# Kernel optimization log

Hardware: AMD Instinct MI355X
Metric: run time of the kernel (lower is better)

## Reference

```python
import jax, jax.numpy as jnp
import numpy as np

BITS = 4
VALS_PER_WORD = 4  # four 4-bit nibbles packed per 16-bit word


def dequantize(w_packed, w_scale, w_bias, dtype):
    # w_packed: [out, groups, cols] int32, each word holds 4 nibbles (little-endian)
    out, g, cols = w_packed.shape
    shifts = jnp.arange(VALS_PER_WORD, dtype=jnp.int32) * BITS  # [4]
    # [out, groups, cols, 4] nibble values in [0, 15]
    q = (w_packed[..., None] >> shifts) & 0xF
    q = q.astype(dtype).reshape(out, g, cols * VALS_PER_WORD)
    w = q * w_scale + w_bias  # per-group affine dequant, scale/bias broadcast over group
    return w.reshape(out, g * cols * VALS_PER_WORD)  # [out, in]


def setup_inputs() -> dict:
    key = jax.random.key(0)
    k1, k2, k3, k4, k5 = jax.random.split(key, 5)
    B, S, IN, OUT, G = 2, 2048, 4096, 16384, 16
    cols = IN // G // VALS_PER_WORD  # 64 packed words per group
    return {
        "input": jax.random.normal(k1, (B, S, IN), dtype=jnp.float32),
        "w_packed": jax.random.randint(k2, (OUT, G, cols), 0, 65536, dtype=jnp.int32),
        "w_scale": jax.random.uniform(k3, (OUT, G, 1), dtype=jnp.float32) * 0.01,
        "w_bias": jax.random.normal(k4, (OUT, G, 1), dtype=jnp.float32) * 0.05,
        "bias": jax.random.normal(k5, (OUT,), dtype=jnp.float32),
    }


def reference(input, w_packed, w_scale, w_bias, bias):
    weight = dequantize(w_packed, w_scale, w_bias, input.dtype)  # [out, in]
    # F.linear: y = x @ W^T + b
    return jnp.einsum("bsi,oi->bso", input, weight) + bias
```

## Files before the change

### kernel.cpp

```cpp
#include <hip/hip_runtime.h>
#include <hip/hip_bf16.h>


typedef short bf16x8 __attribute__((ext_vector_type(8)));
typedef float f32x4 __attribute__((ext_vector_type(4)));
typedef int i32x4 __attribute__((ext_vector_type(4)));
typedef unsigned short u16;
typedef unsigned short u16x8 __attribute__((ext_vector_type(8)));

#define BM 128
#define BN 128
#define BK 64
#define THREADS 256

static __device__ __forceinline__ u16 f2bf(float f) {
    __hip_bfloat16 h = __float2bfloat16(f);
    return __builtin_bit_cast(u16, h);
}


__global__ void rowstat_kernel(const float* __restrict__ x, float* __restrict__ sx,
                               float* __restrict__ rsx, int K) {
    const int m = blockIdx.x;
    const int l = threadIdx.x;
    const float4* p = (const float4*)(x + (size_t)m * K);
    float mx = 0.f;
    for (int i = l; i < (K >> 2); i += 64) {
        const float4 v = p[i];
        mx = fmaxf(mx, fmaxf(fmaxf(fabsf(v.x), fabsf(v.y)),
                             fmaxf(fabsf(v.z), fabsf(v.w))));
    }
    #pragma unroll
    for (int o = 32; o; o >>= 1) mx = fmaxf(mx, __shfl_xor(mx, o));
    if (l == 0) {
        mx = fmaxf(mx, 1e-20f);
        sx[m]  = mx * (1.f / 127.f);
        rsx[m] = 127.f / mx;
    }
}

__global__ void quantX_kernel(const float* __restrict__ x, const float* __restrict__ rsx,
                              char* __restrict__ xq, int kshift, size_t n16) {
    size_t i = (size_t)blockIdx.x * blockDim.x + threadIdx.x;
    if (i >= n16) return;
    const int m = (int)((i * 16) >> kshift);
    const float r = rsx[m];
    const float4* px = (const float4*)(x + i * 16);
    int out[4];
    #pragma unroll
    for (int w = 0; w < 4; ++w) {
        const float4 v = px[w];
        const int b0 = __float2int_rn(v.x * r) & 0xFF;
        const int b1 = __float2int_rn(v.y * r) & 0xFF;
        const int b2 = __float2int_rn(v.z * r) & 0xFF;
        const int b3 = __float2int_rn(v.w * r) & 0xFF;
        out[w] = b0 | (b1 << 8) | (b2 << 16) | (b3 << 24);
    }
    *(int4*)(xq + i * 16) = make_int4(out[0], out[1], out[2], out[3]);
}

__global__ void rowscaleW_kernel(const float* __restrict__ Ws,
                                 const float* __restrict__ Wb,
                                 float* __restrict__ swr, float* __restrict__ rswr,
                                 int G, int N) {
    const int n = blockIdx.x * blockDim.x + threadIdx.x;
    if (n >= N) return;
    float mx = 1e-20f;
    for (int g = 0; g < G; ++g) {
        const float s = Ws[(size_t)n * G + g];
        const float b = Wb[(size_t)n * G + g];
        mx = fmaxf(mx, fmaxf(fabsf(b), fabsf(fmaf(15.f, s, b))));
    }
    swr[n]  = mx * (1.f / 127.f);
    rswr[n] = 127.f / mx;
}

__global__ void quantW_row_kernel(const int* __restrict__ Wp, const float* __restrict__ Ws,
                                  const float* __restrict__ Wb, const float* __restrict__ rswr,
                                  char* __restrict__ wq, int K, int G, int gshift,
                                  int kcshift, size_t nthr) {
    size_t t = (size_t)blockIdx.x * blockDim.x + threadIdx.x;
    if (t >= nthr) return;
    const int n  = (int)(t >> kcshift);
    const int kc = (int)(t & ((1u << kcshift) - 1));
    const int g  = (kc << 4) >> gshift;
    const float s = Ws[(size_t)n * G + g];
    const float b = Wb[(size_t)n * G + g];
    const float rs = rswr[n];
    const int4 wv = *(const int4*)(Wp + (size_t)n * (K >> 2) + ((size_t)kc << 2));
    const int wds[4] = {wv.x, wv.y, wv.z, wv.w};
    int out[4];
    #pragma unroll
    for (int w = 0; w < 4; ++w) {
        int o = 0;
        #pragma unroll
        for (int j = 0; j < 4; ++j) {
            const float v = fmaf((float)((wds[w] >> (4 * j)) & 0xF), s, b);
            o |= (__float2int_rn(v * rs) & 0xFF) << (8 * j);
        }
        out[w] = o;
    }
    *(int4*)(wq + t * 16) = make_int4(out[0], out[1], out[2], out[3]);
}


__global__ __launch_bounds__(512, 2)
void gql_gemm_i8s(const char* __restrict__ xq,
                  const char* __restrict__ wq,
                  const float* __restrict__ swr,
                  const float* __restrict__ sx,
                  const float* __restrict__ Bias,
                  float* __restrict__ Out,
                  int M, int N, int K)
{
    __shared__ __align__(16) char sA[2][256 * 128];
    __shared__ __align__(16) char sB[2][256 * 128];

    const int tid  = threadIdx.x;
    const int lane = tid & 63;
    const int wid  = tid >> 6;
    const int wm   = wid >> 2;
    const int wn   = wid & 3;

    const int nwg = gridDim.x;
    int wg = blockIdx.x;
    if ((nwg & 7) == 0) wg = (wg & 7) * (nwg >> 3) + (wg >> 3);
    const int nt = N / 256;
    const int m0 = (wg / nt) * 256;
    const int n0 = (wg % nt) * 256;

    const int st_row = lane >> 3;
    const int st_g   = ((lane & 7) ^ (lane >> 3)) << 4;

    const int fr = lane & 15;
    const int fq = lane >> 4;

    i32x4 acc[8][4] = {};

    const int NT = K >> 7;

    auto stage = [&](int t, int buf) {
        const size_t k0 = (size_t)t << 7;
        #pragma unroll
        for (int i = 0; i < 4; ++i) {
            const int r = wid * 32 + i * 8 + st_row;
            const char* srcA = xq + (size_t)(m0 + r) * K + k0 + st_g;
            __builtin_amdgcn_global_load_lds(
                (const __attribute__((address_space(1))) void*)srcA,
                (__attribute__((address_space(3))) void*)&sA[buf][(wid * 32 + i * 8) * 128],
                16, 0, 0);
            const char* srcB = wq + (size_t)(n0 + r) * K + k0 + st_g;
            __builtin_amdgcn_global_load_lds(
                (const __attribute__((address_space(1))) void*)srcB,
                (__attribute__((address_space(3))) void*)&sB[buf][(wid * 32 + i * 8) * 128],
                16, 0, 0);
        }
    };

    auto ldsrd = [&](const char* base, int row, int gr) -> i32x4 {
        const u16x8 raw = *(const u16x8*)(base + row * 128 + gr * 16);
        return __builtin_bit_cast(i32x4, raw);
    };

    auto compute = [&](int buf) {
        #pragma unroll
        for (int kk = 0; kk < 2; ++kk) {
            const int gr = (kk * 4 + fq) ^ (fr & 7);
            i32x4 af[8], bfr[4];
            #pragma unroll
            for (int i = 0; i < 8; ++i)
                af[i] = ldsrd(&sA[buf][0], wm * 128 + i * 16 + fr, gr);
            #pragma unroll
            for (int j = 0; j < 4; ++j)
                bfr[j] = ldsrd(&sB[buf][0], wn * 64 + j * 16 + fr, gr);
            __builtin_amdgcn_s_setprio(1);
            #pragma unroll
            for (int i = 0; i < 8; ++i)
                #pragma unroll
                for (int j = 0; j < 4; ++j)
                    acc[i][j] = __builtin_amdgcn_mfma_i32_16x16x64_i8(
                        af[i], bfr[j], acc[i][j], 0, 0, 0);
            __builtin_amdgcn_s_setprio(0);
        }
    };

    stage(0, 0);
    int cur = 0;
    for (int t = 0; t < NT - 1; ++t) {
        stage(t + 1, cur ^ 1);
        __builtin_amdgcn_sched_barrier(0);
        asm volatile("s_waitcnt vmcnt(8)" ::: "memory");
        __builtin_amdgcn_s_barrier();
        asm volatile("" ::: "memory");
        compute(cur);
        __builtin_amdgcn_sched_barrier(0);
        asm volatile("" ::: "memory");
        __builtin_amdgcn_s_barrier();
        asm volatile("" ::: "memory");
        cur ^= 1;
    }
    asm volatile("s_waitcnt vmcnt(0)" ::: "memory");
    __builtin_amdgcn_s_barrier();
    asm volatile("" ::: "memory");
    compute(cur);

    #pragma unroll
    for (int j = 0; j < 4; ++j) {
        const int col = n0 + wn * 64 + j * 16 + fr;
        const float bv = Bias[col];
        const float sv = swr[col];
        #pragma unroll
        for (int i = 0; i < 8; ++i) {
            const int mb = m0 + wm * 128 + i * 16 + (fq << 2);
            #pragma unroll
            for (int r = 0; r < 4; ++r)
                Out[(size_t)(mb + r) * N + col] =
                    fmaf(sx[mb + r] * sv, (float)acc[i][j][r], bv);
        }
    }
}


__global__ void cvtA_kernel(const float* __restrict__ A, u16* __restrict__ wsA,
                            size_t n8) {
    size_t i = (size_t)blockIdx.x * blockDim.x + threadIdx.x;
    if (i >= n8) return;
    const float4 v0 = *(const float4*)(A + i * 8);
    const float4 v1 = *(const float4*)(A + i * 8 + 4);
    u16x8 h;
    h[0] = f2bf(v0.x); h[1] = f2bf(v0.y); h[2] = f2bf(v0.z); h[3] = f2bf(v0.w);
    h[4] = f2bf(v1.x); h[5] = f2bf(v1.y); h[6] = f2bf(v1.z); h[7] = f2bf(v1.w);
    *(u16x8*)(wsA + i * 8) = h;
}

__global__ void deqW_kernel(const int* __restrict__ Wp, const float* __restrict__ Ws,
                            const float* __restrict__ Wb, u16* __restrict__ wsW,
                            int K, int G, int gshift, int kgshift, size_t n8) {
    size_t t = (size_t)blockIdx.x * blockDim.x + threadIdx.x;
    if (t >= n8) return;
    const int n  = (int)(t >> kgshift);
    const int kg = (int)(t & ((1u << kgshift) - 1));
    const int k  = kg << 3;
    const int g  = k >> gshift;
    const float s = Ws[n * G + g];
    const float b = Wb[n * G + g];
    const int2 w2 = *(const int2*)(Wp + (size_t)n * (K >> 2) + (k >> 2));
    u16x8 h;
    #pragma unroll
    for (int j = 0; j < 4; ++j)
        h[j]     = f2bf(fmaf((float)((w2.x >> (4 * j)) & 0xF), s, b));
    #pragma unroll
    for (int j = 0; j < 4; ++j)
        h[4 + j] = f2bf(fmaf((float)((w2.y >> (4 * j)) & 0xF), s, b));
    *(u16x8*)(wsW + ((size_t)n << (kgshift + 3)) + k) = h;
}

__global__ __launch_bounds__(THREADS, 2)
void gql_gemm_pre(const u16* __restrict__ wsA,
                  const u16* __restrict__ wsW,
                  const float* __restrict__ Bias,
                  float* __restrict__ Out,
                  int M, int N, int K)
{
    __shared__ __align__(16) u16 sA[BM * BK];
    __shared__ __align__(16) u16 sB[BN * BK];

    const int tid  = threadIdx.x;
    const int lane = tid & 63;
    const int wid  = tid >> 6;

    const int nwg = gridDim.x;
    int wg = blockIdx.x;
    if ((nwg & 7) == 0) wg = (wg & 7) * (nwg >> 3) + (wg >> 3);
    const int nt     = N / BN;
    const int m0 = (wg / nt) * BM;
    const int n0 = (wg % nt) * BN;

    const int st_r  = (lane >> 3);
    const int st_g  = lane & 7;

    const int wr = (wid >> 1) << 6;
    const int wc = (wid & 1) << 6;
    const int fr = lane & 15;
    const int fq = lane >> 4;

    f32x4 acc[4][4] = {};

    for (int k0 = 0; k0 < K; k0 += BK) {
        __syncthreads();

        #pragma unroll
        for (int i = 0; i < 4; ++i) {
            const int r = wid * 32 + i * 8 + st_r;
            const int gsrc = (st_g ^ (r & 7)) << 3;
            const u16* srcA = wsA + (size_t)(m0 + r) * K + k0 + gsrc;
            const u16* srcB = wsW + (size_t)(n0 + r) * K + k0 + gsrc;
            __builtin_amdgcn_global_load_lds(
                (const __attribute__((address_space(1))) void*)srcA,
                (__attribute__((address_space(3))) void*)&sA[(wid * 32 + i * 8) * BK],
                16, 0, 0);
            __builtin_amdgcn_global_load_lds(
                (const __attribute__((address_space(1))) void*)srcB,
                (__attribute__((address_space(3))) void*)&sB[(wid * 32 + i * 8) * BK],
                16, 0, 0);
        }

        __syncthreads();

        #pragma unroll
        for (int sub = 0; sub < 2; ++sub) {
            const int kch = (sub << 2) + fq;
            bf16x8 af[4], bfg[4];
            #pragma unroll
            for (int i = 0; i < 4; ++i) {
                const int row = wr + i * 16 + fr;
                af[i] = *(const bf16x8*)((const char*)sA + row * (BK * 2)
                                         + (((kch ^ (row & 7)) << 4)));
            }
            #pragma unroll
            for (int j = 0; j < 4; ++j) {
                const int row = wc + j * 16 + fr;
                bfg[j] = *(const bf16x8*)((const char*)sB + row * (BK * 2)
                                          + (((kch ^ (row & 7)) << 4)));
            }
            #pragma unroll
            for (int i = 0; i < 4; ++i)
                #pragma unroll
                for (int j = 0; j < 4; ++j)
                    acc[i][j] = __builtin_amdgcn_mfma_f32_16x16x32_bf16(
                        af[i], bfg[j], acc[i][j], 0, 0, 0);
        }
    }

    #pragma unroll
    for (int j = 0; j < 4; ++j) {
        const int n = n0 + wc + j * 16 + fr;
        const float bvv = Bias[n];
        #pragma unroll
        for (int i = 0; i < 4; ++i) {
            const int mb = m0 + wr + i * 16 + (fq << 2);
            #pragma unroll
            for (int r = 0; r < 4; ++r)
                Out[(size_t)(mb + r) * N + n] = acc[i][j][r] + bvv;
        }
    }
}


__global__ __launch_bounds__(THREADS, 2)
void gql_gemm(const float* __restrict__ A,
              const int* __restrict__ Wp,
              const float* __restrict__ Ws,
              const float* __restrict__ Wb,
              const float* __restrict__ Bias,
              float* __restrict__ Out,
              int M, int N, int K, int G, int gshift)
{
    __shared__ __align__(16) u16 sA[BM * BK];
    __shared__ __align__(16) u16 sB[BN * BK];

    const int tid  = threadIdx.x;
    const int lane = tid & 63;
    const int wid  = tid >> 6;

    const int nwg = gridDim.x;
    int wg = blockIdx.x;
    if ((nwg & 7) == 0) wg = (wg & 7) * (nwg >> 3) + (wg >> 3);
    const int nt     = N / BN;
    const int m0 = (wg / nt) * BM;
    const int n0 = (wg % nt) * BN;

    const int wpr = K >> 2;

    const int a_r = tid >> 4;
    const int a_c = (tid & 15) << 2;
    const int b_r = tid >> 3;
    const int b_w = (tid & 7) << 1;

    const int wr = (wid >> 1) << 6;
    const int wc = (wid & 1) << 6;
    const int fr = lane & 15;
    const int fq = lane >> 4;

    f32x4 acc[4][4] = {};

    for (int k0 = 0; k0 < K; k0 += BK) {
        __syncthreads();

        #pragma unroll
        for (int it = 0; it < 8; ++it) {
            const int row = it * 16 + a_r;
            const float4 v = *(const float4*)(A + (size_t)(m0 + row) * K + (k0 + a_c));
            u16 h0 = f2bf(v.x), h1 = f2bf(v.y), h2 = f2bf(v.z), h3 = f2bf(v.w);
            const int byte = (a_c << 1) ^ ((row & 7) << 4);
            *(u16*)((char*)sA + row * (BK * 2) + byte + 0) = h0;
            *(u16*)((char*)sA + row * (BK * 2) + byte + 2) = h1;
            *(u16*)((char*)sA + row * (BK * 2) + byte + 4) = h2;
            *(u16*)((char*)sA + row * (BK * 2) + byte + 6) = h3;
        }

        const int g = k0 >> gshift;
        #pragma unroll
        for (int it = 0; it < 4; ++it) {
            const int row = it * 32 + b_r;
            const int gn  = n0 + row;
            const int2 w2 = *(const int2*)(Wp + (size_t)gn * wpr + (k0 >> 2) + b_w);
            const float s = Ws[gn * G + g];
            const float b = Wb[gn * G + g];
            u16x8 h;
            #pragma unroll
            for (int j = 0; j < 4; ++j)
                h[j]     = f2bf(fmaf((float)((w2.x >> (4 * j)) & 0xF), s, b));
            #pragma unroll
            for (int j = 0; j < 4; ++j)
                h[4 + j] = f2bf(fmaf((float)((w2.y >> (4 * j)) & 0xF), s, b));
            const int byte = (b_w << 3) ^ ((row & 7) << 4);
            *(u16x8*)((char*)sB + row * (BK * 2) + byte) = h;
        }

        __syncthreads();

        #pragma unroll
        for (int sub = 0; sub < 2; ++sub) {
            const int kch = (sub << 2) + fq;
            bf16x8 af[4], bfg[4];
            #pragma unroll
            for (int i = 0; i < 4; ++i) {
                const int row = wr + i * 16 + fr;
                af[i] = *(const bf16x8*)((const char*)sA + row * (BK * 2)
                                         + ((kch << 4) ^ ((row & 7) << 4)));
            }
            #pragma unroll
            for (int j = 0; j < 4; ++j) {
                const int row = wc + j * 16 + fr;
                bfg[j] = *(const bf16x8*)((const char*)sB + row * (BK * 2)
                                          + ((kch << 4) ^ ((row & 7) << 4)));
            }
            #pragma unroll
            for (int i = 0; i < 4; ++i)
                #pragma unroll
                for (int j = 0; j < 4; ++j)
                    acc[i][j] = __builtin_amdgcn_mfma_f32_16x16x32_bf16(
                        af[i], bfg[j], acc[i][j], 0, 0, 0);
        }
    }

    #pragma unroll
    for (int j = 0; j < 4; ++j) {
        const int n = n0 + wc + j * 16 + fr;
        const float bvv = Bias[n];
        #pragma unroll
        for (int i = 0; i < 4; ++i) {
            const int mb = m0 + wr + i * 16 + (fq << 2);
            #pragma unroll
            for (int r = 0; r < 4; ++r)
                Out[(size_t)(mb + r) * N + n] = acc[i][j][r] + bvv;
        }
    }
}

extern "C" void kernel_launch(void* const* d_in, const int* in_sizes, int n_in,
                              void* d_out, int out_size, void* d_ws, size_t ws_size,
                              hipStream_t stream) {
    const float* A    = (const float*)d_in[0];
    const int*   Wp   = (const int*)d_in[1];
    const float* Ws   = (const float*)d_in[2];
    const float* Wb   = (const float*)d_in[3];
    const float* Bias = (const float*)d_in[4];
    float* Out = (float*)d_out;

    const int OUT  = in_sizes[4];
    const int OG   = in_sizes[2];
    const int G    = OG / OUT;
    const int cols = in_sizes[1] / OG;
    const int IN   = G * cols * 4;
    const int M    = in_sizes[0] / IN;

    const int gk = IN / G;
    int gshift = 0;
    while ((1 << gshift) < gk) ++gshift;

    int kshift = 0;
    while ((1 << kshift) < IN) ++kshift;

    const size_t needXq = (size_t)M * IN;
    const size_t needWq = (size_t)OUT * IN;
    const size_t needSc = (size_t)M * 8 + (size_t)OUT * 8;
    const size_t needI8 = needXq + needWq + needSc;

    const bool kpow2  = ((IN & (IN - 1)) == 0);
    const bool gkpow2 = ((1 << gshift) == gk);

    if (ws_size >= needI8 && kpow2 && gkpow2 && (IN % 128) == 0 && IN >= 256 &&
        (M % 256) == 0 && (OUT % 256) == 0 && (gk % 16) == 0) {
        char*  xq   = (char*)d_ws;
        char*  wq   = (char*)d_ws + needXq;
        float* sx   = (float*)((char*)d_ws + needXq + needWq);
        float* rsx  = sx + M;
        float* swr  = rsx + M;
        float* rswr = swr + OUT;

        rowstat_kernel<<<M, 64, 0, stream>>>(A, sx, rsx, IN);

        const size_t n16 = (size_t)M * IN / 16;
        quantX_kernel<<<(unsigned)((n16 + 255) / 256), 256, 0, stream>>>(
            A, rsx, xq, kshift, n16);

        rowscaleW_kernel<<<(OUT + 255) / 256, 256, 0, stream>>>(Ws, Wb, swr, rswr,
                                                                G, OUT);

        const int kcshift = kshift - 4;
        const size_t nthr = (size_t)OUT * (IN >> 4);
        quantW_row_kernel<<<(unsigned)((nthr + 255) / 256), 256, 0, stream>>>(
            Wp, Ws, Wb, rswr, wq, IN, G, gshift, kcshift, nthr);

        dim3 grid((M / 256) * (OUT / 256));
        gql_gemm_i8s<<<grid, 512, 0, stream>>>(xq, wq, swr, sx, Bias, Out,
                                               M, OUT, IN);
        return;
    }

    const size_t needA = (size_t)M * IN * 2;
    const size_t needW = (size_t)OUT * IN * 2;

    if (ws_size >= needA + needW && (IN & 7) == 0 &&
        (M % 128) == 0 && (OUT % 128) == 0 && (IN % 64) == 0) {
        u16* wsA = (u16*)d_ws;
        u16* wsW = (u16*)((char*)d_ws + needA);

        const size_t nA8 = (size_t)M * IN / 8;
        cvtA_kernel<<<(unsigned)((nA8 + 255) / 256), 256, 0, stream>>>(A, wsA, nA8);

        int kgshift = 0;
        while ((1 << kgshift) < (IN >> 3)) ++kgshift;
        const size_t nW8 = (size_t)OUT * IN / 8;
        deqW_kernel<<<(unsigned)((nW8 + 255) / 256), 256, 0, stream>>>(
            Wp, Ws, Wb, wsW, IN, G, gshift, kgshift, nW8);

        dim3 grid((M / BM) * (OUT / BN));
        gql_gemm_pre<<<grid, THREADS, 0, stream>>>(wsA, wsW, Bias, Out, M, OUT, IN);
    } else {
        dim3 grid((M / BM) * (OUT / BN));
        gql_gemm<<<grid, THREADS, 0, stream>>>(A, Wp, Ws, Wb, Bias, Out,
                                               M, OUT, IN, G, gshift);
    }
}
```

Measured before the change: 370.2 us.

## Switch int8 GEMM to 4-stage K=64 LDS pipeline with split compute phases

Replaces the double-buffered K=128 staging with a four-slot ring of K=64 tiles, prefetching three stages ahead, using a new paired-row swizzled LDS layout. The compute is split into two halves with A fragments reloaded, which lowers register pressure and adds barriers. The goal is to hide global load latency behind more in-flight stages. The cost is more barriers per K step, and redundant tail stage loads once the pipeline reaches the end of K.

Measured after the change: 438.5 us. 18.4% more time.

```diff
diff --git a/kernel.cpp b/kernel.cpp
--- a/kernel.cpp
+++ b/kernel.cpp
@@ -105,7 +105,7 @@
 
 
 __global__ __launch_bounds__(512, 2)
-void gql_gemm_i8s(const char* __restrict__ xq,
+void gql_gemm_i8p(const char* __restrict__ xq,
                   const char* __restrict__ wq,
                   const float* __restrict__ swr,
                   const float* __restrict__ sx,
@@ -113,8 +113,8 @@
                   float* __restrict__ Out,
                   int M, int N, int K)
 {
-    __shared__ __align__(16) char sA[2][256 * 128];
-    __shared__ __align__(16) char sB[2][256 * 128];
+    __shared__ __align__(16) char sA[4][128 * 128];
+    __shared__ __align__(16) char sB[4][128 * 128];
 
     const int tid  = threadIdx.x;
     const int lane = tid & 63;
@@ -129,80 +129,95 @@
     const int m0 = (wg / nt) * 256;
     const int n0 = (wg % nt) * 256;
 
-    const int st_row = lane >> 3;
-    const int st_g   = ((lane & 7) ^ (lane >> 3)) << 4;
-
     const int fr = lane & 15;
     const int fq = lane >> 4;
 
     i32x4 acc[8][4] = {};
 
-    const int NT = K >> 7;
-
-    auto stage = [&](int t, int buf) {
-        const size_t k0 = (size_t)t << 7;
-        #pragma unroll
-        for (int i = 0; i < 4; ++i) {
-            const int r = wid * 32 + i * 8 + st_row;
-            const char* srcA = xq + (size_t)(m0 + r) * K + k0 + st_g;
+    const int NS = K >> 6;
+
+    const int st_row2 = lane >> 3;
+    const int st_q    = lane & 7;
+
+    auto stage = [&](int s, int slot) {
+        const size_t kb = (size_t)s << 6;
+        #pragma unroll
+        for (int i = 0; i < 2; ++i) {
+            const int row2 = wid * 16 + i * 8 + st_row2;
+            const int v    = st_q ^ (row2 & 7);
+            const int r    = 2 * row2 + (v >> 2);
+            const int kc   = v & 3;
+            const size_t goff = kb + (size_t)kc * 16;
+            const char* srcA = xq + (size_t)(m0 + r) * K + goff;
             __builtin_amdgcn_global_load_lds(
                 (const __attribute__((address_space(1))) void*)srcA,
-                (__attribute__((address_space(3))) void*)&sA[buf][(wid * 32 + i * 8) * 128],
+                (__attribute__((address_space(3))) void*)&sA[slot][(wid * 16 + i * 8) * 128],
                 16, 0, 0);
-            const char* srcB = wq + (size_t)(n0 + r) * K + k0 + st_g;
+            const char* srcB = wq + (size_t)(n0 + r) * K + goff;
             __builtin_amdgcn_global_load_lds(
                 (const __attribute__((address_space(1))) void*)srcB,
-                (__attribute__((address_space(3))) void*)&sB[buf][(wid * 32 + i * 8) * 128],
+                (__attribute__((address_space(3))) void*)&sB[slot][(wid * 16 + i * 8) * 128],
                 16, 0, 0);
         }
     };
 
-    auto ldsrd = [&](const char* base, int row, int gr) -> i32x4 {
-        const u16x8 raw = *(const u16x8*)(base + row * 128 + gr * 16);
+    auto ldrd = [&](const char* base, int r) -> i32x4 {
+        const int row2 = r >> 1;
+        const int q = (fq + ((r & 1) << 2)) ^ (row2 & 7);
+        const u16x8 raw = *(const u16x8*)(base + row2 * 128 + q * 16);
         return __builtin_bit_cast(i32x4, raw);
     };
 
-    auto compute = [&](int buf) {
-        #pragma unroll
-        for (int kk = 0; kk < 2; ++kk) {
-            const int gr = (kk * 4 + fq) ^ (fr & 7);
-            i32x4 af[8], bfr[4];
-            #pragma unroll
-            for (int i = 0; i < 8; ++i)
-                af[i] = ldsrd(&sA[buf][0], wm * 128 + i * 16 + fr, gr);
-            #pragma unroll
-            for (int j = 0; j < 4; ++j)
-                bfr[j] = ldsrd(&sB[buf][0], wn * 64 + j * 16 + fr, gr);
-            __builtin_amdgcn_s_setprio(1);
-            #pragma unroll
-            for (int i = 0; i < 8; ++i)
-                #pragma unroll
-                for (int j = 0; j < 4; ++j)
-                    acc[i][j] = __builtin_amdgcn_mfma_i32_16x16x64_i8(
-                        af[i], bfr[j], acc[i][j], 0, 0, 0);
-            __builtin_amdgcn_s_setprio(0);
-        }
-    };
-
-    stage(0, 0);
-    int cur = 0;
-    for (int t = 0; t < NT - 1; ++t) {
-        stage(t + 1, cur ^ 1);
+    stage(0, 0); stage(1, 1); stage(2, 2);
+
+    for (int s = 0; s < NS; ++s) {
+        const int slot = s & 3;
+        const int sn = (s + 3 < NS) ? (s + 3) : (NS - 1);
+        stage(sn, (s + 3) & 3);
         __builtin_amdgcn_sched_barrier(0);
-        asm volatile("s_waitcnt vmcnt(8)" ::: "memory");
+        asm volatile("s_waitcnt vmcnt(12)" ::: "memory");
         __builtin_amdgcn_s_barrier();
         asm volatile("" ::: "memory");
-        compute(cur);
+
+        i32x4 a4[4], bfr[4];
+
+        #pragma unroll
+        for (int i = 0; i < 4; ++i)
+            a4[i] = ldrd(&sA[slot][0], wm * 128 + i * 16 + fr);
+        #pragma unroll
+        for (int j = 0; j < 4; ++j)
+            bfr[j] = ldrd(&sB[slot][0], wn * 64 + j * 16 + fr);
+        asm volatile("s_waitcnt lgkmcnt(0)" ::: "memory");
         __builtin_amdgcn_sched_barrier(0);
-        asm volatile("" ::: "memory");
+        __builtin_amdgcn_s_setprio(1);
+        #pragma unroll
+        for (int i = 0; i < 4; ++i)
+            #pragma unroll
+            for (int j = 0; j < 4; ++j)
+                acc[i][j] = __builtin_amdgcn_mfma_i32_16x16x64_i8(
+                    a4[i], bfr[j], acc[i][j], 0, 0, 0);
+        __builtin_amdgcn_s_setprio(0);
         __builtin_amdgcn_s_barrier();
         asm volatile("" ::: "memory");
-        cur ^= 1;
-    }
+
+        #pragma unroll
+        for (int i = 0; i < 4; ++i)
+            a4[i] = ldrd(&sA[slot][0], wm * 128 + (i + 4) * 16 + fr);
+        asm volatile("s_waitcnt lgkmcnt(0)" ::: "memory");
+        __builtin_amdgcn_sched_barrier(0);
+        __builtin_amdgcn_s_setprio(1);
+        #pragma unroll
+        for (int i = 0; i < 4; ++i)
+            #pragma unroll
+            for (int j = 0; j < 4; ++j)
+                acc[i + 4][j] = __builtin_amdgcn_mfma_i32_16x16x64_i8(
+                    a4[i], bfr[j], acc[i + 4][j], 0, 0, 0);
+        __builtin_amdgcn_s_setprio(0);
+        __builtin_amdgcn_s_barrier();
+        asm volatile("" ::: "memory");
+    }
+
     asm volatile("s_waitcnt vmcnt(0)" ::: "memory");
-    __builtin_amdgcn_s_barrier();
-    asm volatile("" ::: "memory");
-    compute(cur);
 
     #pragma unroll
     for (int j = 0; j < 4; ++j) {
@@ -491,7 +506,7 @@
     const bool kpow2  = ((IN & (IN - 1)) == 0);
     const bool gkpow2 = ((1 << gshift) == gk);
 
-    if (ws_size >= needI8 && kpow2 && gkpow2 && (IN % 128) == 0 && IN >= 256 &&
+    if (ws_size >= needI8 && kpow2 && gkpow2 && (IN % 256) == 0 &&
         (M % 256) == 0 && (OUT % 256) == 0 && (gk % 16) == 0) {
         char*  xq   = (char*)d_ws;
         char*  wq   = (char*)d_ws + needXq;
@@ -515,7 +530,7 @@
             Wp, Ws, Wb, rswr, wq, IN, G, gshift, kcshift, nthr);
 
         dim3 grid((M / 256) * (OUT / 256));
-        gql_gemm_i8s<<<grid, 512, 0, stream>>>(xq, wq, swr, sx, Bias, Out,
+        gql_gemm_i8p<<<grid, 512, 0, stream>>>(xq, wq, swr, sx, Bias, Out,
                                                M, OUT, IN);
         return;
     }
```

## Shrink int8 GEMM tile to 256x128 with 4 waves and BK=64

Applied to the files above, without the earlier changes.

Replaces the 256x256x128 int8 GEMM tile run by 8 waves with a 256x128x64 tile run by 4 waves, each wave still computing a 128x64 sub-tile. LDS staging and the XOR swizzle are rewritten for 64-byte rows, and the vmcnt wait count is adjusted to match. This cuts LDS per block and doubles the grid, aiming at better occupancy and load balance. In exchange, each tile reuses its operands less and the kernel synchronizes twice as often along K.

After: 388.4 us. 1.05x slower.

```diff
diff --git a/kernel.cpp b/kernel.cpp
--- a/kernel.cpp
+++ b/kernel.cpp
@@ -104,8 +104,8 @@
 }
 
 
-__global__ __launch_bounds__(512, 2)
-void gql_gemm_i8s(const char* __restrict__ xq,
+__global__ __launch_bounds__(256, 2)
+void gql_gemm_i8t(const char* __restrict__ xq,
                   const char* __restrict__ wq,
                   const float* __restrict__ swr,
                   const float* __restrict__ sx,
@@ -113,75 +113,80 @@
                   float* __restrict__ Out,
                   int M, int N, int K)
 {
-    __shared__ __align__(16) char sA[2][256 * 128];
-    __shared__ __align__(16) char sB[2][256 * 128];
+    __shared__ __align__(16) char sA[2][256 * 64];
+    __shared__ __align__(16) char sB[2][128 * 64];
 
     const int tid  = threadIdx.x;
     const int lane = tid & 63;
     const int wid  = tid >> 6;
-    const int wm   = wid >> 2;
-    const int wn   = wid & 3;
+    const int wm   = wid >> 1;
+    const int wn   = wid & 1;
 
     const int nwg = gridDim.x;
     int wg = blockIdx.x;
     if ((nwg & 7) == 0) wg = (wg & 7) * (nwg >> 3) + (wg >> 3);
-    const int nt = N / 256;
+    const int nt = N / 128;
     const int m0 = (wg / nt) * 256;
-    const int n0 = (wg % nt) * 256;
-
-    const int st_row = lane >> 3;
-    const int st_g   = ((lane & 7) ^ (lane >> 3)) << 4;
+    const int n0 = (wg % nt) * 128;
 
     const int fr = lane & 15;
     const int fq = lane >> 4;
 
+    const int st_kc  = ((lane & 3) ^ ((lane >> 3) & 3)) << 4;
+    const int st_rw  = lane >> 2;
+
+    const int rq = (fq ^ ((fr >> 1) & 3)) << 4;
+
     i32x4 acc[8][4] = {};
 
-    const int NT = K >> 7;
+    const int NT = K >> 6;
 
     auto stage = [&](int t, int buf) {
-        const size_t k0 = (size_t)t << 7;
+        const size_t k0 = (size_t)t << 6;
         #pragma unroll
         for (int i = 0; i < 4; ++i) {
-            const int r = wid * 32 + i * 8 + st_row;
-            const char* srcA = xq + (size_t)(m0 + r) * K + k0 + st_g;
+            const int inst = wid + i * 4;
+            const int row  = inst * 16 + st_rw;
+            const char* src = xq + (size_t)(m0 + row) * K + k0 + st_kc;
             __builtin_amdgcn_global_load_lds(
-                (const __attribute__((address_space(1))) void*)srcA,
-                (__attribute__((address_space(3))) void*)&sA[buf][(wid * 32 + i * 8) * 128],
+                (const __attribute__((address_space(1))) void*)src,
+                (__attribute__((address_space(3))) void*)&sA[buf][inst * 1024],
                 16, 0, 0);
-            const char* srcB = wq + (size_t)(n0 + r) * K + k0 + st_g;
+        }
+        #pragma unroll
+        for (int i = 0; i < 2; ++i) {
+            const int inst = wid + i * 4;
+            const int row  = inst * 16 + st_rw;
+            const char* src = wq + (size_t)(n0 + row) * K + k0 + st_kc;
             __builtin_amdgcn_global_load_lds(
-                (const __attribute__((address_space(1))) void*)srcB,
-                (__attribute__((address_space(3))) void*)&sB[buf][(wid * 32 + i * 8) * 128],
+                (const __attribute__((address_space(1))) void*)src,
+                (__attribute__((address_space(3))) void*)&sB[buf][inst * 1024],
                 16, 0, 0);
         }
     };
 
-    auto ldsrd = [&](const char* base, int row, int gr) -> i32x4 {
-        const u16x8 raw = *(const u16x8*)(base + row * 128 + gr * 16);
-        return __builtin_bit_cast(i32x4, raw);
-    };
-
     auto compute = [&](int buf) {
-        #pragma unroll
-        for (int kk = 0; kk < 2; ++kk) {
-            const int gr = (kk * 4 + fq) ^ (fr & 7);
-            i32x4 af[8], bfr[4];
-            #pragma unroll
-            for (int i = 0; i < 8; ++i)
-                af[i] = ldsrd(&sA[buf][0], wm * 128 + i * 16 + fr, gr);
+        i32x4 af[8], bfr[4];
+        #pragma unroll
+        for (int i = 0; i < 8; ++i) {
+            const int row = wm * 128 + i * 16 + fr;
+            const u16x8 raw = *(const u16x8*)(&sA[buf][row * 64 + rq]);
+            af[i] = __builtin_bit_cast(i32x4, raw);
+        }
+        #pragma unroll
+        for (int j = 0; j < 4; ++j) {
+            const int row = wn * 64 + j * 16 + fr;
+            const u16x8 raw = *(const u16x8*)(&sB[buf][row * 64 + rq]);
+            bfr[j] = __builtin_bit_cast(i32x4, raw);
+        }
+        __builtin_amdgcn_s_setprio(1);
+        #pragma unroll
+        for (int i = 0; i < 8; ++i)
             #pragma unroll
             for (int j = 0; j < 4; ++j)
-                bfr[j] = ldsrd(&sB[buf][0], wn * 64 + j * 16 + fr, gr);
-            __builtin_amdgcn_s_setprio(1);
-            #pragma unroll
-            for (int i = 0; i < 8; ++i)
-                #pragma unroll
-                for (int j = 0; j < 4; ++j)
-                    acc[i][j] = __builtin_amdgcn_mfma_i32_16x16x64_i8(
-                        af[i], bfr[j], acc[i][j], 0, 0, 0);
-            __builtin_amdgcn_s_setprio(0);
-        }
+                acc[i][j] = __builtin_amdgcn_mfma_i32_16x16x64_i8(
+                    af[i], bfr[j], acc[i][j], 0, 0, 0);
+        __builtin_amdgcn_s_setprio(0);
     };
 
     stage(0, 0);
@@ -189,7 +194,7 @@
     for (int t = 0; t < NT - 1; ++t) {
         stage(t + 1, cur ^ 1);
         __builtin_amdgcn_sched_barrier(0);
-        asm volatile("s_waitcnt vmcnt(8)" ::: "memory");
+        asm volatile("s_waitcnt vmcnt(6)" ::: "memory");
         __builtin_amdgcn_s_barrier();
         asm volatile("" ::: "memory");
         compute(cur);
@@ -491,8 +496,8 @@
     const bool kpow2  = ((IN & (IN - 1)) == 0);
     const bool gkpow2 = ((1 << gshift) == gk);
 
-    if (ws_size >= needI8 && kpow2 && gkpow2 && (IN % 128) == 0 && IN >= 256 &&
-        (M % 256) == 0 && (OUT % 256) == 0 && (gk % 16) == 0) {
+    if (ws_size >= needI8 && kpow2 && gkpow2 && (IN % 256) == 0 &&
+        (M % 256) == 0 && (OUT % 128) == 0 && (gk % 16) == 0) {
         char*  xq   = (char*)d_ws;
         char*  wq   = (char*)d_ws + needXq;
         float* sx   = (float*)((char*)d_ws + needXq + needWq);
@@ -514,8 +519,8 @@
         quantW_row_kernel<<<(unsigned)((nthr + 255) / 256), 256, 0, stream>>>(
             Wp, Ws, Wb, rswr, wq, IN, G, gshift, kcshift, nthr);
 
-        dim3 grid((M / 256) * (OUT / 256));
-        gql_gemm_i8s<<<grid, 512, 0, stream>>>(xq, wq, swr, sx, Bias, Out,
+        dim3 grid((M / 256) * (OUT / 128));
+        gql_gemm_i8t<<<grid, 256, 0, stream>>>(xq, wq, swr, sx, Bias, Out,
                                                M, OUT, IN);
         return;
     }
```

## Interleave half-tile prefetch with quarter-tile MFMA phases in int8 GEMM main loop

Applied to the files above, without the earlier changes.

Restructures the int8 GEMM main loop into a two-tile unrolled schedule. Each K tile is split into four compute phases of 4x4 MFMAs. The global-to-LDS staging for the next tile is split into halves and issued between phases. A-fragment register use is cut to 4 at a time, which may lower register pressure, but every phase adds an LDS wait and a block barrier, and the loop now requires K to be a multiple of 256.

After: 409.3 us. +10.6%, slower.

```diff
diff --git a/kernel.cpp b/kernel.cpp
--- a/kernel.cpp
+++ b/kernel.cpp
@@ -104,8 +104,13 @@
 }
 
 
+#define LGKM0() do { asm volatile("s_waitcnt lgkmcnt(0)" ::: "memory"); \
+                     __builtin_amdgcn_sched_barrier(0); } while (0)
+#define BARRIER() do { __builtin_amdgcn_s_barrier(); \
+                       asm volatile("" ::: "memory"); } while (0)
+
 __global__ __launch_bounds__(512, 2)
-void gql_gemm_i8s(const char* __restrict__ xq,
+void gql_gemm_i8v(const char* __restrict__ xq,
                   const char* __restrict__ wq,
                   const float* __restrict__ swr,
                   const float* __restrict__ sx,
@@ -129,20 +134,21 @@
     const int m0 = (wg / nt) * 256;
     const int n0 = (wg % nt) * 256;
 
+    const int fr = lane & 15;
+    const int fq = lane >> 4;
+
     const int st_row = lane >> 3;
     const int st_g   = ((lane & 7) ^ (lane >> 3)) << 4;
 
-    const int fr = lane & 15;
-    const int fq = lane >> 4;
-
     i32x4 acc[8][4] = {};
 
     const int NT = K >> 7;
-
-    auto stage = [&](int t, int buf) {
+    const int NI = NT >> 1;
+
+    auto stage_half = [&](int t, int buf, int h) {
         const size_t k0 = (size_t)t << 7;
         #pragma unroll
-        for (int i = 0; i < 4; ++i) {
+        for (int i = h * 2; i < h * 2 + 2; ++i) {
             const int r = wid * 32 + i * 8 + st_row;
             const char* srcA = xq + (size_t)(m0 + r) * K + k0 + st_g;
             __builtin_amdgcn_global_load_lds(
@@ -157,52 +163,133 @@
         }
     };
 
-    auto ldsrd = [&](const char* base, int row, int gr) -> i32x4 {
-        const u16x8 raw = *(const u16x8*)(base + row * 128 + gr * 16);
-        return __builtin_bit_cast(i32x4, raw);
+    auto rd = [&](const char* bA, const char* bB, int kk, int ih,
+                  i32x4* af, i32x4* bfr, bool loadB) {
+        const int gr = (((kk << 2) + fq) ^ (fr & 7)) << 4;
+        #pragma unroll
+        for (int i = 0; i < 4; ++i) {
+            const int row = wm * 128 + (ih * 4 + i) * 16 + fr;
+            af[i] = __builtin_bit_cast(i32x4, *(const u16x8*)(bA + row * 128 + gr));
+        }
+        if (loadB) {
+            #pragma unroll
+            for (int j = 0; j < 4; ++j) {
+                const int row = wn * 64 + j * 16 + fr;
+                bfr[j] = __builtin_bit_cast(i32x4, *(const u16x8*)(bB + row * 128 + gr));
+            }
+        }
     };
 
-    auto compute = [&](int buf) {
-        #pragma unroll
-        for (int kk = 0; kk < 2; ++kk) {
-            const int gr = (kk * 4 + fq) ^ (fr & 7);
-            i32x4 af[8], bfr[4];
-            #pragma unroll
-            for (int i = 0; i < 8; ++i)
-                af[i] = ldsrd(&sA[buf][0], wm * 128 + i * 16 + fr, gr);
-            #pragma unroll
-            for (int j = 0; j < 4; ++j)
-                bfr[j] = ldsrd(&sB[buf][0], wn * 64 + j * 16 + fr, gr);
-            __builtin_amdgcn_s_setprio(1);
-            #pragma unroll
-            for (int i = 0; i < 8; ++i)
-                #pragma unroll
-                for (int j = 0; j < 4; ++j)
-                    acc[i][j] = __builtin_amdgcn_mfma_i32_16x16x64_i8(
-                        af[i], bfr[j], acc[i][j], 0, 0, 0);
-            __builtin_amdgcn_s_setprio(0);
-        }
-    };
-
-    stage(0, 0);
-    int cur = 0;
-    for (int t = 0; t < NT - 1; ++t) {
-        stage(t + 1, cur ^ 1);
+    const char* bA0 = &sA[0][0]; const char* bB0 = &sB[0][0];
+    const char* bA1 = &sA[1][0]; const char* bB1 = &sB[1][0];
+
+    stage_half(0, 0, 0); stage_half(0, 0, 1);
+
+    for (int u = 0; u < NI; ++u) {
+        const int t1  = 2 * u + 1;
+        const int tn0 = (2 * u + 2 < NT) ? 2 * u + 2 : NT - 1;
+        i32x4 af[4], bfr[4];
+
+        asm volatile("s_waitcnt vmcnt(0)" ::: "memory");
         __builtin_amdgcn_sched_barrier(0);
-        asm volatile("s_waitcnt vmcnt(8)" ::: "memory");
-        __builtin_amdgcn_s_barrier();
-        asm volatile("" ::: "memory");
-        compute(cur);
+        BARRIER();
+        stage_half(t1, 1, 0);
+        rd(bA0, bB0, 0, 0, af, bfr, true);
+        LGKM0();
+        __builtin_amdgcn_s_setprio(1);
+        #pragma unroll
+        for (int i = 0; i < 4; ++i)
+            #pragma unroll
+            for (int j = 0; j < 4; ++j)
+                acc[i][j] = __builtin_amdgcn_mfma_i32_16x16x64_i8(af[i], bfr[j], acc[i][j], 0, 0, 0);
+        __builtin_amdgcn_s_setprio(0);
+        BARRIER();
+
+        stage_half(t1, 1, 1);
+        rd(bA0, bB0, 0, 1, af, bfr, false);
+        LGKM0();
+        __builtin_amdgcn_s_setprio(1);
+        #pragma unroll
+        for (int i = 0; i < 4; ++i)
+            #pragma unroll
+            for (int j = 0; j < 4; ++j)
+                acc[4 + i][j] = __builtin_amdgcn_mfma_i32_16x16x64_i8(af[i], bfr[j], acc[4 + i][j], 0, 0, 0);
+        __builtin_amdgcn_s_setprio(0);
+        BARRIER();
+
+        rd(bA0, bB0, 1, 0, af, bfr, true);
+        LGKM0();
+        __builtin_amdgcn_s_setprio(1);
+        #pragma unroll
+        for (int i = 0; i < 4; ++i)
+            #pragma unroll
+            for (int j = 0; j < 4; ++j)
+                acc[i][j] = __builtin_amdgcn_mfma_i32_16x16x64_i8(af[i], bfr[j], acc[i][j], 0, 0, 0);
+        __builtin_amdgcn_s_setprio(0);
+        BARRIER();
+
+        rd(bA0, bB0, 1, 1, af, bfr, false);
+        LGKM0();
+        __builtin_amdgcn_s_setprio(1);
+        #pragma unroll
+        for (int i = 0; i < 4; ++i)
+            #pragma unroll
+            for (int j = 0; j < 4; ++j)
+                acc[4 + i][j] = __builtin_amdgcn_mfma_i32_16x16x64_i8(af[i], bfr[j], acc[4 + i][j], 0, 0, 0);
+        __builtin_amdgcn_s_setprio(0);
+        BARRIER();
+
+        asm volatile("s_waitcnt vmcnt(0)" ::: "memory");
         __builtin_amdgcn_sched_barrier(0);
-        asm volatile("" ::: "memory");
-        __builtin_amdgcn_s_barrier();
-        asm volatile("" ::: "memory");
-        cur ^= 1;
-    }
+        BARRIER();
+        stage_half(tn0, 0, 0);
+        rd(bA1, bB1, 0, 0, af, bfr, true);
+        LGKM0();
+        __builtin_amdgcn_s_setprio(1);
+        #pragma unroll
+        for (int i = 0; i < 4; ++i)
+            #pragma unroll
+            for (int j = 0; j < 4; ++j)
+                acc[i][j] = __builtin_amdgcn_mfma_i32_16x16x64_i8(af[i], bfr[j], acc[i][j], 0, 0, 0);
+        __builtin_amdgcn_s_setprio(0);
+        BARRIER();
+
+        stage_half(tn0, 0, 1);
+        rd(bA1, bB1, 0, 1, af, bfr, false);
+        LGKM0();
+        __builtin_amdgcn_s_setprio(1);
+        #pragma unroll
+        for (int i = 0; i < 4; ++i)
+            #pragma unroll
+            for (int j = 0; j < 4; ++j)
+                acc[4 + i][j] = __builtin_amdgcn_mfma_i32_16x16x64_i8(af[i], bfr[j], acc[4 + i][j], 0, 0, 0);
+        __builtin_amdgcn_s_setprio(0);
+        BARRIER();
+
+        rd(bA1, bB1, 1, 0, af, bfr, true);
+        LGKM0();
+        __builtin_amdgcn_s_setprio(1);
+        #pragma unroll
+        for (int i = 0; i < 4; ++i)
+            #pragma unroll
+            for (int j = 0; j < 4; ++j)
+                acc[i][j] = __builtin_amdgcn_mfma_i32_16x16x64_i8(af[i], bfr[j], acc[i][j], 0, 0, 0);
+        __builtin_amdgcn_s_setprio(0);
+        BARRIER();
+
+        rd(bA1, bB1, 1, 1, af, bfr, false);
+        LGKM0();
+        __builtin_amdgcn_s_setprio(1);
+        #pragma unroll
+        for (int i = 0; i < 4; ++i)
+            #pragma unroll
+            for (int j = 0; j < 4; ++j)
+                acc[4 + i][j] = __builtin_amdgcn_mfma_i32_16x16x64_i8(af[i], bfr[j], acc[4 + i][j], 0, 0, 0);
+        __builtin_amdgcn_s_setprio(0);
+        BARRIER();
+    }
+
     asm volatile("s_waitcnt vmcnt(0)" ::: "memory");
-    __builtin_amdgcn_s_barrier();
-    asm volatile("" ::: "memory");
-    compute(cur);
 
     #pragma unroll
     for (int j = 0; j < 4; ++j) {
@@ -491,7 +578,7 @@
     const bool kpow2  = ((IN & (IN - 1)) == 0);
     const bool gkpow2 = ((1 << gshift) == gk);
 
-    if (ws_size >= needI8 && kpow2 && gkpow2 && (IN % 128) == 0 && IN >= 256 &&
+    if (ws_size >= needI8 && kpow2 && gkpow2 && (IN % 256) == 0 &&
         (M % 256) == 0 && (OUT % 256) == 0 && (gk % 16) == 0) {
         char*  xq   = (char*)d_ws;
         char*  wq   = (char*)d_ws + needXq;
@@ -515,7 +602,7 @@
             Wp, Ws, Wb, rswr, wq, IN, G, gshift, kcshift, nthr);
 
         dim3 grid((M / 256) * (OUT / 256));
-        gql_gemm_i8s<<<grid, 512, 0, stream>>>(xq, wq, swr, sx, Bias, Out,
+        gql_gemm_i8v<<<grid, 512, 0, stream>>>(xq, wq, swr, sx, Bias, Out,
                                                M, OUT, IN);
         return;
     }
```
